# Kernel optimization log

Hardware: AMD Instinct MI355X
Metric: run time of the kernel (lower is better)

Reference implementation:

```python
import jax, jax.numpy as jnp
import numpy as np

B, S, IN = 8, 512, 128
D, H, DK, DV, DFF, L = 512, 8, 64, 64, 2048, 4
LOCAL = 64
EPS = 1e-5


def setup_inputs() -> dict:
    key = jax.random.key(0)
    ks = jax.random.split(key, 12)
    w = lambda k, shape: (jax.random.normal(k, shape, jnp.float32) * 0.02)
    return dict(
        x=jax.random.normal(ks[0], (B, S, IN), jnp.float32),
        We=w(ks[1], (IN, D)), be=jnp.zeros((D,), jnp.float32),
        Wq=w(ks[2], (L, D, H * DK)), bq=jnp.zeros((L, H * DK), jnp.float32),
        Wk=w(ks[3], (L, D, H * DK)), bk=jnp.zeros((L, H * DK), jnp.float32),
        Wv=w(ks[4], (L, D, H * DV)), bv=jnp.zeros((L, H * DV), jnp.float32),
        Wo=w(ks[5], (L, H * DV, D)), bo=jnp.zeros((L, D), jnp.float32),
        ln1_g=jnp.ones((L, D), jnp.float32), ln1_b=jnp.zeros((L, D), jnp.float32),
        W1=w(ks[6], (L, D, DFF)), b1=jnp.zeros((L, DFF), jnp.float32),
        W2=w(ks[7], (L, DFF, D)), b2=jnp.zeros((L, D), jnp.float32),
        ln2_g=jnp.ones((L, D), jnp.float32), ln2_b=jnp.zeros((L, D), jnp.float32),
    )


def _layernorm(x, g, b):
    m = jnp.mean(x, -1, keepdims=True)
    v = jnp.mean((x - m) ** 2, -1, keepdims=True)
    return (x - m) / jnp.sqrt(v + EPS) * g + b


def _gelu(x):
    # GELU tanh approximation exactly as in the torch module
    return 0.5 * x * (1.0 + jnp.tanh(np.sqrt(2.0 / np.pi) * (x + 0.044715 * x ** 3)))


def _sincos_pe():
    pos = jnp.arange(S, dtype=jnp.float32)[:, None]
    div = jnp.exp(jnp.arange(0, D, 2, dtype=jnp.float32) * (-np.log(10000.0) / D))
    pe = jnp.zeros((S, D), jnp.float32)
    pe = pe.at[:, 0::2].set(jnp.sin(pos * div))
    pe = pe.at[:, 1::2].set(jnp.cos(pos * div))
    return pe


def _forward(x, We, be, Wq, bq, Wk, bk, Wv, bv, Wo, bo,
             ln1_g, ln1_b, W1, b1, W2, b2, ln2_g, ln2_b):
    h = x @ We + be + _sincos_pe()  # [B,S,D]
    idx = jnp.arange(S)
    # local band mask: positions farther than LOCAL are masked with -1e9
    mask = jnp.abs(idx[:, None] - idx[None, :]) > LOCAL  # [S,S] bool

    def mha(hin, l):
        q = (hin @ Wq[l] + bq[l]).reshape(B, S, H, DK).transpose(0, 2, 1, 3)
        k = (hin @ Wk[l] + bk[l]).reshape(B, S, H, DK).transpose(0, 2, 1, 3)
        v = (hin @ Wv[l] + bv[l]).reshape(B, S, H, DV).transpose(0, 2, 1, 3)
        scores = jnp.einsum('bhqd,bhkd->bhqk', q, k) / np.sqrt(DK)
        scores = jnp.where(mask, -1e9, scores)
        a = jax.nn.softmax(scores, axis=-1)
        ctx = jnp.einsum('bhqk,bhkd->bhqd', a, v)
        ctx = ctx.transpose(0, 2, 1, 3).reshape(B, S, H * DV)
        out = ctx @ Wo[l] + bo[l]
        return _layernorm(out + hin, ln1_g[l], ln1_b[l]), a

    attns = []
    for l in range(L):
        h, a = mha(h, l)
        h, a = mha(h, l)  # local=True: second pass with the SAME weights
        ff = _gelu(h @ W1[l] + b1[l]) @ W2[l] + b2[l]
        h = _layernorm(ff + h, ln2_g[l], ln2_b[l])
        attns.append(a)
    attns = jnp.stack(attns).transpose(1, 0, 2, 3, 4)  # [B,L,H,S,S]
    return h, attns


def reference(x, We, be, Wq, bq, Wk, bk, Wv, bv, Wo, bo,
              ln1_g, ln1_b, W1, b1, W2, b2, ln2_g, ln2_b):
    return _forward(x, We, be, Wq, bq, Wk, bk, Wv, bv, Wo, bo,
                    ln1_g, ln1_b, W1, b1, W2, b2, ln2_g, ln2_b)
```

## Files before the change

kernel.cpp:

```cpp
#include <hip/hip_runtime.h>

using bf16 = __bf16;
using bf16x8 = __attribute__((ext_vector_type(8))) __bf16;
using bf16x4 = __attribute__((ext_vector_type(4))) __bf16;
using f32x4  = __attribute__((ext_vector_type(4))) float;

#define AS1(p) ((const __attribute__((address_space(1))) unsigned int*)(p))
#define AS3(p) ((__attribute__((address_space(3))) unsigned int*)(p))

template<int N> __device__ __forceinline__ void wait_vmcnt() {
    if constexpr (N == 0) asm volatile("s_waitcnt vmcnt(0)" ::: "memory");
    else if constexpr (N == 2) asm volatile("s_waitcnt vmcnt(2)" ::: "memory");
    else if constexpr (N == 3) asm volatile("s_waitcnt vmcnt(3)" ::: "memory");
    else if constexpr (N == 4) asm volatile("s_waitcnt vmcnt(4)" ::: "memory");
    else if constexpr (N == 6) asm volatile("s_waitcnt vmcnt(6)" ::: "memory");
    else if constexpr (N == 8) asm volatile("s_waitcnt vmcnt(8)" ::: "memory");
}

template<int TM, int TN, int EPI>
__global__ __launch_bounds__(256, 4)
void gemm_kernel(const bf16* __restrict__ A, const bf16* __restrict__ WT,
                 const float* __restrict__ bias, bf16* __restrict__ Cbf,
                 float* __restrict__ Cf, const float* __restrict__ PE,
                 int K, int ldc, int gx, int q8)
{
    constexpr int NA  = TM / 16;
    constexpr int NCH = NA + TN / 16;
    constexpr int CPW = NCH / 4;
    constexpr int MI  = TM / 32;
    constexpr int NI  = TN / 32;
    constexpr int ASZ = TM * 32;
    constexpr int BSZ = TN * 32;
    __shared__ bf16 Asm[3 * ASZ];
    __shared__ bf16 Bsm[3 * BSZ];
    const int tid = threadIdx.x;
    const int lane = tid & 63;
    const int w  = tid >> 6;
    const int wr = w >> 1, wc = w & 1;
    const int l4 = lane & 15, lg = lane >> 4;

    const int bid = blockIdx.x;
    const int s  = (bid & 7) * q8 + (bid >> 3);
    const int by = s / gx, bx = s - by * gx;
    const size_t m0 = (size_t)by * TM;
    const size_t n0 = (size_t)bx * TN;

    f32x4 acc[MI][NI] = {};

    const int lr  = lane >> 2;
    const int ksw = (((lane & 3) ^ ((lane >> 3) & 3)) * 8);
    const bf16* src[CPW];
    bf16* dst0[CPW];
    int step[CPW];
    #pragma unroll
    for (int ci = 0; ci < CPW; ++ci) {
        const int c = w * CPW + ci;
        if (c < NA) {
            src[ci]  = A + (m0 + (size_t)(c * 16 + lr)) * K + ksw;
            dst0[ci] = Asm + c * 512;
            step[ci] = ASZ;
        } else {
            src[ci]  = WT + (n0 + (size_t)((c - NA) * 16 + lr)) * K + ksw;
            dst0[ci] = Bsm + (c - NA) * 512;
            step[ci] = BSZ;
        }
    }
    const int rsw = (lg ^ ((l4 >> 1) & 3)) * 8;
    const bf16* Ar = &Asm[(wr * (TM / 2) + l4) * 32 + rsw];
    const bf16* Br = &Bsm[(wc * (TN / 2) + l4) * 32 + rsw];

    auto STAGE = [&](int b) {
        #pragma unroll
        for (int ci = 0; ci < CPW; ++ci) {
            __builtin_amdgcn_global_load_lds(AS1(src[ci]),
                                             AS3(dst0[ci] + b * step[ci]), 16, 0, 0);
            src[ci] += 32;
        }
    };

    const int nt = K >> 5;
    STAGE(0);
    if (nt > 1) STAGE(1);

    int cur = 0;
    for (int t = 0; t < nt; ++t) {
        if (t + 2 < nt) {
            int pb = cur - 1; if (pb < 0) pb = 2;
            STAGE(pb);
            wait_vmcnt<2 * CPW>();
        } else if (t + 1 < nt) {
            wait_vmcnt<CPW>();
        } else {
            wait_vmcnt<0>();
        }
        __builtin_amdgcn_s_barrier();
        const bf16* Ac = Ar + cur * ASZ;
        const bf16* Bc = Br + cur * BSZ;
        bf16x8 aF[MI], bF[NI];
        #pragma unroll
        for (int i = 0; i < MI; ++i) aF[i] = *(const bf16x8*)(Ac + i * 512);
        #pragma unroll
        for (int i = 0; i < NI; ++i) bF[i] = *(const bf16x8*)(Bc + i * 512);
        #pragma unroll
        for (int mi = 0; mi < MI; ++mi)
            #pragma unroll
            for (int ni = 0; ni < NI; ++ni)
                acc[mi][ni] = __builtin_amdgcn_mfma_f32_16x16x32_bf16(
                    aF[mi], bF[ni], acc[mi][ni], 0, 0, 0);
        asm volatile("s_waitcnt lgkmcnt(0)" ::: "memory");
        __builtin_amdgcn_s_barrier();
        cur = (cur == 2) ? 0 : cur + 1;
    }

    #pragma unroll
    for (int ni = 0; ni < NI; ++ni) {
        const int col = (int)n0 + wc * (TN / 2) + ni * 16 + l4;
        const float bv = bias[col];
        #pragma unroll
        for (int mi = 0; mi < MI; ++mi) {
            const int row0 = (int)m0 + wr * (TM / 2) + mi * 16 + lg * 4;
            #pragma unroll
            for (int r = 0; r < 4; ++r) {
                float v = acc[mi][ni][r] + bv;
                const int row = row0 + r;
                if (EPI == 1) {
                    float u = 1.5957691216057308f * (v + 0.044715f * v * v * v);
                    v = v / (1.0f + __expf(-u));
                }
                if (EPI == 2) {
                    v += PE[((row & 511) << 9) + col];
                    Cf[(size_t)row * ldc + col] = v;
                }
                Cbf[(size_t)row * ldc + col] = (bf16)v;
            }
        }
    }
}

template<int WRITE_ATTN>
__global__ __launch_bounds__(256, 3)
void attn_kernel(const bf16* __restrict__ qkv, bf16* __restrict__ ctx,
                 float* __restrict__ attn_out )
{
    __shared__ bf16 KPs[192 * 72];
    __shared__ bf16 Vt[64 * 200];
    bf16* Ks = KPs;
    bf16* Ps = KPs;
    const int tid = threadIdx.x;
    const int lane = tid & 63, w = tid >> 6;
    const int l4 = lane & 15, lg = lane >> 4;
    const int bh = blockIdx.y, ib = blockIdx.x;
    const int b = bh >> 3, hd = bh & 7;
    const int i0 = ib * 64;
    const int j0 = (i0 >= 64) ? i0 - 64 : 0;
    const int j1 = (i0 + 128 <= 512) ? i0 + 128 : 512;
    const int W = j1 - j0;
    const size_t rowb = (size_t)b * 512;

    if (WRITE_ATTN) {
        float* arow = attn_out + (size_t)b * 8388608 + (size_t)hd * 262144 +
                      (size_t)i0 * 512;
        const int zr = tid >> 2, p = tid & 3;
        f32x4 z = {0.f, 0.f, 0.f, 0.f};
        f32x4* rp = (f32x4*)(arow + (size_t)zr * 512);
        for (int c = p; c < (j0 >> 2); c += 4) rp[c] = z;
        for (int c = (j1 >> 2) + p; c < 128; c += 4) rp[c] = z;
    }

    for (int it = 0; it < 6; ++it) {
        int chunk = tid + it * 256;
        int j = chunk >> 3, k0 = (chunk & 7) * 8;
        if (j < W) {
            bf16x8 v = *(const bf16x8*)(qkv + (rowb + j0 + j) * 1536 + 512 + hd * 64 + k0);
            *(bf16x8*)(&Ks[j * 72 + k0]) = v;
        }
    }
    for (int it = 0; it < 6; ++it) {
        int chunk = tid + it * 256;
        int j = chunk >> 3, d0 = (chunk & 7) * 8;
        if (j < W) {
            bf16x8 v = *(const bf16x8*)(qkv + (rowb + j0 + j) * 1536 + 1024 + hd * 64 + d0);
            #pragma unroll
            for (int e = 0; e < 8; ++e) Vt[(d0 + e) * 200 + j] = v[e];
        }
    }
    bf16x8 qF0, qF1;
    {
        const bf16* qrow = qkv + (rowb + i0 + w * 16 + l4) * 1536 + hd * 64;
        qF0 = *(const bf16x8*)(qrow + lg * 8);
        qF1 = *(const bf16x8*)(qrow + 32 + lg * 8);
    }
    __syncthreads();

    f32x4 s[12];
    #pragma unroll
    for (int t = 0; t < 12; ++t) s[t] = (f32x4){0.f, 0.f, 0.f, 0.f};
    const int NT = W >> 4;
    __builtin_amdgcn_s_setprio(1);
    for (int t = 0; t < NT; ++t) {
        const bf16* kb = &Ks[(t * 16 + l4) * 72];
        bf16x8 b0 = *(const bf16x8*)(kb + lg * 8);
        bf16x8 b1 = *(const bf16x8*)(kb + 32 + lg * 8);
        s[t] = __builtin_amdgcn_mfma_f32_16x16x32_bf16(qF0, b0, s[t], 0, 0, 0);
        s[t] = __builtin_amdgcn_mfma_f32_16x16x32_bf16(qF1, b1, s[t], 0, 0, 0);
    }
    __builtin_amdgcn_s_setprio(0);
    const int irow0 = i0 + w * 16 + lg * 4;
    float pm[4] = {-3e38f, -3e38f, -3e38f, -3e38f};
    for (int t = 0; t < NT; ++t) {
        int jg = j0 + t * 16 + l4;
        #pragma unroll
        for (int r = 0; r < 4; ++r) {
            int dd = irow0 + r - jg;
            float sv = s[t][r] * 0.125f;
            if (dd > 64 || dd < -64) sv = -1e30f;
            s[t][r] = sv;
            pm[r] = fmaxf(pm[r], sv);
        }
    }
    #pragma unroll
    for (int d = 1; d < 16; d <<= 1)
        #pragma unroll
        for (int r = 0; r < 4; ++r) pm[r] = fmaxf(pm[r], __shfl_xor(pm[r], d));
    float ps[4] = {0.f, 0.f, 0.f, 0.f};
    for (int t = 0; t < NT; ++t)
        #pragma unroll
        for (int r = 0; r < 4; ++r) {
            float p = __expf(s[t][r] - pm[r]);
            s[t][r] = p;
            ps[r] += p;
        }
    #pragma unroll
    for (int d = 1; d < 16; d <<= 1)
        #pragma unroll
        for (int r = 0; r < 4; ++r) ps[r] += __shfl_xor(ps[r], d);
    float rinv[4];
    #pragma unroll
    for (int r = 0; r < 4; ++r) rinv[r] = 1.0f / ps[r];

    __syncthreads();

    for (int t = 0; t < NT; ++t) {
        #pragma unroll
        for (int r = 0; r < 4; ++r) {
            float p = s[t][r] * rinv[r];
            Ps[(w * 16 + lg * 4 + r) * 200 + t * 16 + l4] = (bf16)p;
            if (WRITE_ATTN) {
                size_t off = (size_t)b * 8388608 + (size_t)hd * 262144 +
                             (size_t)(i0 + w * 16 + lg * 4 + r) * 512 +
                             (size_t)(j0 + t * 16 + l4);
                attn_out[off] = p;
            }
        }
    }
    f32x4 o[4] = {};
    const int KS = W >> 5;
    __builtin_amdgcn_s_setprio(1);
    for (int ks = 0; ks < KS; ++ks) {
        bf16x8 aF = *(const bf16x8*)(&Ps[(w * 16 + l4) * 200 + ks * 32 + lg * 8]);
        #pragma unroll
        for (int ni = 0; ni < 4; ++ni) {
            bf16x8 bF = *(const bf16x8*)(&Vt[(ni * 16 + l4) * 200 + ks * 32 + lg * 8]);
            o[ni] = __builtin_amdgcn_mfma_f32_16x16x32_bf16(aF, bF, o[ni], 0, 0, 0);
        }
    }
    __builtin_amdgcn_s_setprio(0);
    __syncthreads();
    bf16* Cs = Vt;
    #pragma unroll
    for (int ni = 0; ni < 4; ++ni)
        #pragma unroll
        for (int r = 0; r < 4; ++r)
            Cs[(w * 16 + lg * 4 + r) * 64 + ni * 16 + l4] = (bf16)o[ni][r];
    __syncthreads();
    #pragma unroll
    for (int it = 0; it < 2; ++it) {
        int chunk = tid + it * 256;
        int rl = chunk >> 3, c0 = (chunk & 7) << 3;
        *(bf16x8*)(&ctx[(rowb + i0 + rl) * 512 + hd * 64 + c0]) =
            *(const bf16x8*)(&Cs[rl * 64 + c0]);
    }
}

__global__ __launch_bounds__(256)
void ln_kernel(const bf16* __restrict__ y, const float* hin,
               const float* __restrict__ g, const float* __restrict__ bb,
               float* hf, bf16* __restrict__ hbf)
{
    const int row = blockIdx.x * 4 + (threadIdx.x >> 6);
    const int lane = threadIdx.x & 63;
    const size_t base = (size_t)row * 512 + lane * 8;
    bf16x8 yv = *(const bf16x8*)(y + base);
    f32x4 h0 = *(const f32x4*)(hin + base);
    f32x4 h1 = *(const f32x4*)(hin + base + 4);
    float x[8];
    #pragma unroll
    for (int i = 0; i < 8; ++i) x[i] = (float)yv[i] + (i < 4 ? h0[i] : h1[i - 4]);
    float s = 0.f, q = 0.f;
    #pragma unroll
    for (int i = 0; i < 8; ++i) { s += x[i]; q += x[i] * x[i]; }
    #pragma unroll
    for (int d = 1; d < 64; d <<= 1) { s += __shfl_xor(s, d); q += __shfl_xor(q, d); }
    const float m = s * 0.001953125f;
    const float var = q * 0.001953125f - m * m;
    const float rstd = rsqrtf(var + 1e-5f);
    const int c0 = lane * 8;
    f32x4 g0 = *(const f32x4*)(g + c0), g1v = *(const f32x4*)(g + c0 + 4);
    f32x4 b0 = *(const f32x4*)(bb + c0), b1v = *(const f32x4*)(bb + c0 + 4);
    f32x4 o0, o1;
    bf16x8 ob;
    #pragma unroll
    for (int i = 0; i < 8; ++i) {
        float gg = i < 4 ? g0[i] : g1v[i - 4];
        float bv = i < 4 ? b0[i] : b1v[i - 4];
        float o = (x[i] - m) * rstd * gg + bv;
        if (i < 4) o0[i] = o; else o1[i - 4] = o;
        ob[i] = (bf16)o;
    }
    *(f32x4*)(hf + base) = o0;
    *(f32x4*)(hf + base + 4) = o1;
    *(bf16x8*)(hbf + base) = ob;
}

struct TMat { const float* src; size_t dst; int K; int N; int tile0; };
struct TDesc { TMat m[26]; };

__global__ __launch_bounds__(256)
void wtrans_kernel(TDesc d, bf16* __restrict__ wbuf)
{
    __shared__ float tile[32][33];
    int t = blockIdx.x;
    int mi = 0;
    while (t >= d.m[mi + 1].tile0) ++mi;
    const TMat mm = d.m[mi];
    const int lt = t - mm.tile0;
    const int tpr = mm.N >> 5;
    const int kt = lt / tpr, nt = lt % tpr;
    const int r = threadIdx.x >> 5, c = threadIdx.x & 31;
    #pragma unroll
    for (int it = 0; it < 4; ++it)
        tile[r + it * 8][c] =
            mm.src[(size_t)(kt * 32 + r + it * 8) * mm.N + nt * 32 + c];
    __syncthreads();
    #pragma unroll
    for (int it = 0; it < 4; ++it)
        wbuf[mm.dst + (size_t)(nt * 32 + r + it * 8) * mm.K + kt * 32 + c] =
            (bf16)tile[c][r + it * 8];
}

__global__ void prep_kernel(const float* __restrict__ x, bf16* __restrict__ xbf,
                            float* __restrict__ pe,
                            const float* bq, const float* bk, const float* bv,
                            float* __restrict__ bqkv)
{
    const int bid = blockIdx.x;
    if (bid < 512) {
        int i = bid * 256 + threadIdx.x;
        f32x4 v = *(const f32x4*)(x + (size_t)i * 4);
        bf16x4 o;
        #pragma unroll
        for (int e = 0; e < 4; ++e) o[e] = (bf16)v[e];
        *(bf16x4*)(xbf + (size_t)i * 4) = o;
    } else if (bid < 1024) {
        int i = (bid - 512) * 256 + threadIdx.x;
        int s = i >> 8, d2 = i & 255;
        float ang = (float)s * expf((float)(2 * d2) * -0.017988946039016f);
        pe[(s << 9) + 2 * d2]     = sinf(ang);
        pe[(s << 9) + 2 * d2 + 1] = cosf(ang);
    } else {
        int i = (bid - 1024) * 256 + threadIdx.x;
        if (i < 6144) {
            int l = i / 1536, c = i - l * 1536;
            float v;
            if (c < 512) v = bq[l * 512 + c];
            else if (c < 1024) v = bk[l * 512 + c - 512];
            else v = bv[l * 512 + c - 1024];
            bqkv[i] = v;
        }
    }
}

extern "C" void kernel_launch(void* const* d_in, const int* in_sizes, int n_in,
                              void* d_out, int out_size, void* d_ws, size_t ws_size,
                              hipStream_t stream)
{
    const float* x   = (const float*)d_in[0];
    const float* We  = (const float*)d_in[1];
    const float* be  = (const float*)d_in[2];
    const float* Wq  = (const float*)d_in[3];
    const float* bq  = (const float*)d_in[4];
    const float* Wk  = (const float*)d_in[5];
    const float* bk  = (const float*)d_in[6];
    const float* Wv  = (const float*)d_in[7];
    const float* bv  = (const float*)d_in[8];
    const float* Wo  = (const float*)d_in[9];
    const float* bo  = (const float*)d_in[10];
    const float* g1  = (const float*)d_in[11];
    const float* b1n = (const float*)d_in[12];
    const float* W1  = (const float*)d_in[13];
    const float* b1f = (const float*)d_in[14];
    const float* W2  = (const float*)d_in[15];
    const float* b2f = (const float*)d_in[16];
    const float* g2  = (const float*)d_in[17];
    const float* b2n = (const float*)d_in[18];

    char* ws = (char*)d_ws;
    bf16* wbuf = (bf16*)ws;
    size_t off = 12648448ull * 2;
    float* bqkv = (float*)(ws + off); off += 6144ull * 4;
    float* pe   = (float*)(ws + off); off += 262144ull * 4;
    bf16* xbf   = (bf16*)(ws + off);  off += 524288ull * 2;
    float* h    = (float*)(ws + off); off += 2097152ull * 4;
    bf16* hbf   = (bf16*)(ws + off);  off += 2097152ull * 2;
    bf16* qkvb  = (bf16*)(ws + off);  off += 6291456ull * 2;
    bf16* ctx   = (bf16*)(ws + off);  off += 2097152ull * 2;
    bf16* tmp   = (bf16*)(ws + off);  off += 2097152ull * 2;
    bf16* ffn   = (bf16*)(ws + off);  off += 8388608ull * 2;
    (void)ws_size; (void)in_sizes; (void)n_in; (void)out_size;

    float* out_h = (float*)d_out;
    float* out_attn = out_h + 2097152;

    TDesc td{};
    int tile = 0, e = 0;
    auto add = [&](const float* src, size_t dst, int K, int N) {
        td.m[e].src = src; td.m[e].dst = dst; td.m[e].K = K; td.m[e].N = N;
        td.m[e].tile0 = tile; tile += (K >> 5) * (N >> 5); ++e;
    };
    add(We, 0, 128, 512);
    for (int l = 0; l < 4; ++l) {
        size_t base = 65536 + (size_t)l * 3145728;
        add(Wq + (size_t)l * 262144,  base + 0,       512, 512);
        add(Wk + (size_t)l * 262144,  base + 262144,  512, 512);
        add(Wv + (size_t)l * 262144,  base + 524288,  512, 512);
        add(Wo + (size_t)l * 262144,  base + 786432,  512, 512);
        add(W1 + (size_t)l * 1048576, base + 1048576, 512, 2048);
        add(W2 + (size_t)l * 1048576, base + 2097152, 2048, 512);
    }
    td.m[e].tile0 = tile;

    wtrans_kernel<<<dim3(tile), dim3(256), 0, stream>>>(td, wbuf);
    prep_kernel<<<dim3(1048), dim3(256), 0, stream>>>(x, xbf, pe, bq, bk, bv, bqkv);

    gemm_kernel<64, 64, 2><<<dim3(512), dim3(256), 0, stream>>>(
        xbf, wbuf, be, hbf, h, pe, 128, 512, 8, 64);

    for (int l = 0; l < 4; ++l) {
        const bf16* WqkvT = wbuf + 65536 + (size_t)l * 3145728;
        const bf16* WoT   = WqkvT + 786432;
        const bf16* W1T   = WqkvT + 1048576;
        const bf16* W2T   = WqkvT + 2097152;
        for (int pass = 0; pass < 2; ++pass) {
            gemm_kernel<64, 128, 0><<<dim3(768), dim3(256), 0, stream>>>(
                hbf, WqkvT, bqkv + l * 1536, qkvb, (float*)nullptr, (float*)nullptr,
                512, 1536, 12, 96);
            if (pass == 0)
                attn_kernel<0><<<dim3(8, 64), dim3(256), 0, stream>>>(
                    qkvb, ctx, (float*)nullptr);
            else
                attn_kernel<1><<<dim3(8, 64), dim3(256), 0, stream>>>(
                    qkvb, ctx, out_attn + (size_t)l * 2097152);
            gemm_kernel<64, 64, 0><<<dim3(512), dim3(256), 0, stream>>>(
                ctx, WoT, bo + l * 512, tmp, (float*)nullptr, (float*)nullptr,
                512, 512, 8, 64);
            ln_kernel<<<dim3(1024), dim3(256), 0, stream>>>(
                tmp, h, g1 + l * 512, b1n + l * 512, h, hbf);
        }
        gemm_kernel<64, 128, 1><<<dim3(1024), dim3(256), 0, stream>>>(
            hbf, W1T, b1f + l * 2048, ffn, (float*)nullptr, (float*)nullptr,
            512, 2048, 16, 128);
        gemm_kernel<64, 64, 0><<<dim3(512), dim3(256), 0, stream>>>(
            ffn, W2T, b2f + l * 512, tmp, (float*)nullptr, (float*)nullptr,
            2048, 512, 8, 64);
        float* hout = (l == 3) ? out_h : h;
        ln_kernel<<<dim3(1024), dim3(256), 0, stream>>>(
            tmp, h, g2 + l * 512, b2n + l * 512, hout, hbf);
    }
}
```

Before: 710.4 us.

## Drop fp32 residual stream, keep residual in bf16, enlarge GEMM tiles

Removes the fp32 hidden-state buffer, so the residual is read and written only as bf16 in the layernorm kernel, and the fp32 copy is written only for the final output. GEMM tile sizes change to 128x128 for the QKV and W1 projections and 64x128 for Wo and W2, with grid sizes and launch bounds adjusted to match. This cuts memory traffic and the number of blocks launched. In exchange the residual stream accumulates bf16 rounding across layers, which risks accuracy, and fewer blocks may reduce occupancy on the smaller GEMMs.

```diff
diff --git a/kernel.cpp b/kernel.cpp
--- a/kernel.cpp
+++ b/kernel.cpp
@@ -10,7 +10,6 @@
 
 template<int N> __device__ __forceinline__ void wait_vmcnt() {
     if constexpr (N == 0) asm volatile("s_waitcnt vmcnt(0)" ::: "memory");
-    else if constexpr (N == 2) asm volatile("s_waitcnt vmcnt(2)" ::: "memory");
     else if constexpr (N == 3) asm volatile("s_waitcnt vmcnt(3)" ::: "memory");
     else if constexpr (N == 4) asm volatile("s_waitcnt vmcnt(4)" ::: "memory");
     else if constexpr (N == 6) asm volatile("s_waitcnt vmcnt(6)" ::: "memory");
@@ -18,10 +17,10 @@
 }
 
 template<int TM, int TN, int EPI>
-__global__ __launch_bounds__(256, 4)
+__global__ __launch_bounds__(256, TM == 64 ? 4 : 3)
 void gemm_kernel(const bf16* __restrict__ A, const bf16* __restrict__ WT,
                  const float* __restrict__ bias, bf16* __restrict__ Cbf,
-                 float* __restrict__ Cf, const float* __restrict__ PE,
+                 const float* __restrict__ PE,
                  int K, int ldc, int gx, int q8)
 {
     constexpr int NA  = TM / 16;
@@ -129,7 +128,6 @@
                 }
                 if (EPI == 2) {
                     v += PE[((row & 511) << 9) + col];
-                    Cf[(size_t)row * ldc + col] = v;
                 }
                 Cbf[(size_t)row * ldc + col] = (bf16)v;
             }
@@ -283,19 +281,18 @@
 }
 
 __global__ __launch_bounds__(256)
-void ln_kernel(const bf16* __restrict__ y, const float* hin,
+void ln_kernel(const bf16* __restrict__ y, const bf16* __restrict__ hin,
                const float* __restrict__ g, const float* __restrict__ bb,
-               float* hf, bf16* __restrict__ hbf)
+               bf16* __restrict__ hbf, float* __restrict__ hf)
 {
     const int row = blockIdx.x * 4 + (threadIdx.x >> 6);
     const int lane = threadIdx.x & 63;
     const size_t base = (size_t)row * 512 + lane * 8;
     bf16x8 yv = *(const bf16x8*)(y + base);
-    f32x4 h0 = *(const f32x4*)(hin + base);
-    f32x4 h1 = *(const f32x4*)(hin + base + 4);
+    bf16x8 hv = *(const bf16x8*)(hin + base);
     float x[8];
     #pragma unroll
-    for (int i = 0; i < 8; ++i) x[i] = (float)yv[i] + (i < 4 ? h0[i] : h1[i - 4]);
+    for (int i = 0; i < 8; ++i) x[i] = (float)yv[i] + (float)hv[i];
     float s = 0.f, q = 0.f;
     #pragma unroll
     for (int i = 0; i < 8; ++i) { s += x[i]; q += x[i] * x[i]; }
@@ -307,19 +304,25 @@
     const int c0 = lane * 8;
     f32x4 g0 = *(const f32x4*)(g + c0), g1v = *(const f32x4*)(g + c0 + 4);
     f32x4 b0 = *(const f32x4*)(bb + c0), b1v = *(const f32x4*)(bb + c0 + 4);
-    f32x4 o0, o1;
-    bf16x8 ob;
+    float o[8];
     #pragma unroll
     for (int i = 0; i < 8; ++i) {
         float gg = i < 4 ? g0[i] : g1v[i - 4];
         float bv = i < 4 ? b0[i] : b1v[i - 4];
-        float o = (x[i] - m) * rstd * gg + bv;
-        if (i < 4) o0[i] = o; else o1[i - 4] = o;
-        ob[i] = (bf16)o;
-    }
-    *(f32x4*)(hf + base) = o0;
-    *(f32x4*)(hf + base + 4) = o1;
-    *(bf16x8*)(hbf + base) = ob;
+        o[i] = (x[i] - m) * rstd * gg + bv;
+    }
+    if (hf) {
+        f32x4 o0, o1;
+        #pragma unroll
+        for (int i = 0; i < 4; ++i) { o0[i] = o[i]; o1[i] = o[i + 4]; }
+        *(f32x4*)(hf + base) = o0;
+        *(f32x4*)(hf + base + 4) = o1;
+    } else {
+        bf16x8 ob;
+        #pragma unroll
+        for (int i = 0; i < 8; ++i) ob[i] = (bf16)o[i];
+        *(bf16x8*)(hbf + base) = ob;
+    }
 }
 
 struct TMat { const float* src; size_t dst; int K; int N; int tile0; };
@@ -410,7 +413,6 @@
     float* bqkv = (float*)(ws + off); off += 6144ull * 4;
     float* pe   = (float*)(ws + off); off += 262144ull * 4;
     bf16* xbf   = (bf16*)(ws + off);  off += 524288ull * 2;
-    float* h    = (float*)(ws + off); off += 2097152ull * 4;
     bf16* hbf   = (bf16*)(ws + off);  off += 2097152ull * 2;
     bf16* qkvb  = (bf16*)(ws + off);  off += 6291456ull * 2;
     bf16* ctx   = (bf16*)(ws + off);  off += 2097152ull * 2;
@@ -442,8 +444,8 @@
     wtrans_kernel<<<dim3(tile), dim3(256), 0, stream>>>(td, wbuf);
     prep_kernel<<<dim3(1048), dim3(256), 0, stream>>>(x, xbf, pe, bq, bk, bv, bqkv);
 
-    gemm_kernel<64, 64, 2><<<dim3(512), dim3(256), 0, stream>>>(
-        xbf, wbuf, be, hbf, h, pe, 128, 512, 8, 64);
+    gemm_kernel<64, 128, 2><<<dim3(256), dim3(256), 0, stream>>>(
+        xbf, wbuf, be, hbf, pe, 128, 512, 4, 32);
 
     for (int l = 0; l < 4; ++l) {
         const bf16* WqkvT = wbuf + 65536 + (size_t)l * 3145728;
@@ -451,29 +453,29 @@
         const bf16* W1T   = WqkvT + 1048576;
         const bf16* W2T   = WqkvT + 2097152;
         for (int pass = 0; pass < 2; ++pass) {
-            gemm_kernel<64, 128, 0><<<dim3(768), dim3(256), 0, stream>>>(
-                hbf, WqkvT, bqkv + l * 1536, qkvb, (float*)nullptr, (float*)nullptr,
-                512, 1536, 12, 96);
+            gemm_kernel<128, 128, 0><<<dim3(384), dim3(256), 0, stream>>>(
+                hbf, WqkvT, bqkv + l * 1536, qkvb, (float*)nullptr,
+                512, 1536, 12, 48);
             if (pass == 0)
                 attn_kernel<0><<<dim3(8, 64), dim3(256), 0, stream>>>(
                     qkvb, ctx, (float*)nullptr);
             else
                 attn_kernel<1><<<dim3(8, 64), dim3(256), 0, stream>>>(
                     qkvb, ctx, out_attn + (size_t)l * 2097152);
-            gemm_kernel<64, 64, 0><<<dim3(512), dim3(256), 0, stream>>>(
-                ctx, WoT, bo + l * 512, tmp, (float*)nullptr, (float*)nullptr,
-                512, 512, 8, 64);
+            gemm_kernel<64, 128, 0><<<dim3(256), dim3(256), 0, stream>>>(
+                ctx, WoT, bo + l * 512, tmp, (float*)nullptr,
+                512, 512, 4, 32);
             ln_kernel<<<dim3(1024), dim3(256), 0, stream>>>(
-                tmp, h, g1 + l * 512, b1n + l * 512, h, hbf);
-        }
-        gemm_kernel<64, 128, 1><<<dim3(1024), dim3(256), 0, stream>>>(
-            hbf, W1T, b1f + l * 2048, ffn, (float*)nullptr, (float*)nullptr,
-            512, 2048, 16, 128);
-        gemm_kernel<64, 64, 0><<<dim3(512), dim3(256), 0, stream>>>(
-            ffn, W2T, b2f + l * 512, tmp, (float*)nullptr, (float*)nullptr,
-            2048, 512, 8, 64);
-        float* hout = (l == 3) ? out_h : h;
+                tmp, hbf, g1 + l * 512, b1n + l * 512, hbf, (float*)nullptr);
+        }
+        gemm_kernel<128, 128, 1><<<dim3(512), dim3(256), 0, stream>>>(
+            hbf, W1T, b1f + l * 2048, ffn, (float*)nullptr,
+            512, 2048, 16, 64);
+        gemm_kernel<64, 128, 0><<<dim3(256), dim3(256), 0, stream>>>(
+            ffn, W2T, b2f + l * 512, tmp, (float*)nullptr,
+            2048, 512, 4, 32);
         ln_kernel<<<dim3(1024), dim3(256), 0, stream>>>(
-            tmp, h, g2 + l * 512, b2n + l * 512, hout, hbf);
-    }
-}
+            tmp, hbf, g2 + l * 512, b2n + l * 512, hbf,
+            (l == 3) ? out_h : (float*)nullptr);
+    }
+}
```

Measured after the change: 673.4 us. 5.2% less time.
